# Kernel optimization log

Measured on AMD Instinct MI355X. Metric: run time of the kernel, lower is better.

Reference implementation:

```python
import jax, jax.numpy as jnp
import numpy as np

HEADS = 8
DIM_HEAD = 64


def setup_inputs() -> dict:
    key = jax.random.key(0)
    ks = jax.random.split(key, 7)
    b, c, h, w = 8, 256, 64, 64
    hidden = HEADS * DIM_HEAD  # 512
    return {
        "x": jax.random.normal(ks[0], (b, c, h, w), dtype=jnp.float32),
        "context": jax.random.normal(ks[1], (b, c, h, w), dtype=jnp.float32),
        "Wq": jax.random.normal(ks[2], (hidden, c), dtype=jnp.float32) * 0.02,
        "Wk": jax.random.normal(ks[3], (hidden, c), dtype=jnp.float32) * 0.02,
        "Wv": jax.random.normal(ks[4], (hidden, c), dtype=jnp.float32) * 0.02,
        "Wo": jax.random.normal(ks[5], (c, hidden), dtype=jnp.float32) * 0.02,
        "bo": jnp.zeros((c,), dtype=jnp.float32),
    }


def reference(x, context, Wq, Wk, Wv, Wo, bo):
    b, c, h, w = x.shape
    n = h * w
    scale = DIM_HEAD ** (-0.5)
    xf = x.reshape(b, c, n)                      # b c n
    cf = context.reshape(b, context.shape[1], -1)  # b c m
    # 1x1 convs == per-pixel linear projections
    q = jnp.einsum('bcn,oc->bon', xf, Wq).reshape(b, HEADS, DIM_HEAD, n) * scale
    k = jnp.einsum('bcm,oc->bom', cf, Wk).reshape(b, HEADS, DIM_HEAD, -1)
    v = jnp.einsum('bcm,oc->bom', cf, Wv).reshape(b, HEADS, DIM_HEAD, -1)
    k = jax.nn.softmax(k, axis=-1)               # softmax over spatial positions
    ctx = jnp.einsum('bhdm,bhem->bhde', k, v)    # small d x e context
    out = jnp.einsum('bhde,bhdn->bhen', ctx, q)  # b h e n
    out = out.reshape(b, HEADS * DIM_HEAD, h, w)
    return jnp.einsum('bchw,oc->bohw', out, Wo) + bo[None, :, None, None]
```

## Files before the change

### kernel.cpp

```cpp
#include <hip/hip_runtime.h>

#define B   8
#define C   256
#define N   4096
#define H   8
#define D   64
#define HID 512
#define SCALE 0.125f

typedef __attribute__((ext_vector_type(8))) __bf16 bf16x8;
typedef __attribute__((ext_vector_type(4))) float f32x4;

__device__ __forceinline__ ushort f2bf(float f) {
  union { float f; unsigned u; } v; v.f = f;
  unsigned r = v.u + 0x7FFFu + ((v.u >> 16) & 1u);
  return (ushort)(r >> 16);
}

__device__ __forceinline__ f32x4 mfma16(bf16x8 a, bf16x8 b, f32x4 c) {
  return __builtin_amdgcn_mfma_f32_16x16x32_bf16(a, b, c, 0, 0, 0);
}

__device__ __forceinline__ void glds16(const ushort* g, ushort* l) {
  __builtin_amdgcn_global_load_lds(
      (const __attribute__((address_space(1))) void*)g,
      (__attribute__((address_space(3))) void*)l, 16, 0, 0);
}

__global__ __launch_bounds__(256) void prep_kernel(
    const float* __restrict__ x, const float* __restrict__ ctxt,
    const float* __restrict__ Wk, const float* __restrict__ Wv,
    ushort* __restrict__ x_bf, ushort* __restrict__ ctxt_bf,
    ushort* __restrict__ wk_bf, ushort* __restrict__ wv_bf) {
  const int z = blockIdx.z;
  if (z == 16) {
    const int id = blockIdx.y * 64 + blockIdx.x;
    if (id >= 128) return;
    const int t = (id * 256 + threadIdx.x) * 4;
    const float4 a = *(const float4*)(Wk + t);
    const float4 b = *(const float4*)(Wv + t);
    ushort4 ra, rb;
    ra.x = f2bf(a.x); ra.y = f2bf(a.y); ra.z = f2bf(a.z); ra.w = f2bf(a.w);
    rb.x = f2bf(b.x); rb.y = f2bf(b.y); rb.z = f2bf(b.z); rb.w = f2bf(b.w);
    *(ushort4*)(wk_bf + t) = ra;
    *(ushort4*)(wv_bf + t) = rb;
    return;
  }
  __shared__ float tile[64 * 65];
  const int b = z & 7;
  const float* src = (z < 8) ? ctxt : x;
  ushort* dst = (z < 8) ? ctxt_bf : x_bf;
  const int l0 = blockIdx.x * 64, r0 = blockIdx.y * 64;
  const int tid = threadIdx.x;
  const int rr = tid >> 4, c4 = (tid & 15) << 2;
  const float* sp = src + ((size_t)b * C + r0) * N + l0;
#pragma unroll
  for (int p = 0; p < 4; ++p) {
    const float4 v = *(const float4*)(sp + (size_t)(rr + p * 16) * N + c4);
    float* tp = tile + (rr + p * 16) * 65 + c4;
    tp[0] = v.x; tp[1] = v.y; tp[2] = v.z; tp[3] = v.w;
  }
  __syncthreads();
  const int lr = tid >> 2, rb = (tid & 3) << 4;
  uint pk[8];
#pragma unroll
  for (int k = 0; k < 16; k += 2) {
    const uint lo = f2bf(tile[(rb + k) * 65 + lr]);
    const uint hi = f2bf(tile[(rb + k + 1) * 65 + lr]);
    pk[k >> 1] = lo | (hi << 16);
  }
  ushort* dp = dst + ((size_t)b * N + l0 + lr) * C + r0 + rb;
  *(uint4*)dp = *(uint4*)pk;
  *(uint4*)(dp + 8) = *(uint4*)(pk + 4);
}

__global__ __launch_bounds__(256, 4) void kv_mfma_kernel(
    const ushort* __restrict__ ctxt_bf,
    const ushort* __restrict__ wk_bf,
    const ushort* __restrict__ wv_bf,
    float* __restrict__ ctx_part,
    float* __restrict__ z_part)
{
  __shared__ __align__(16) ushort cb_s[2][32 * 256];
  __shared__ __align__(16) ushort p_s[64 * 32];
  __shared__ __align__(16) ushort v_s[64 * 32];
  const int mt = blockIdx.x, h = blockIdx.y, b = blockIdx.z;
  const int tid = threadIdx.x;
  const int w = tid >> 6, lane = tid & 63;
  const int col = lane & 15, quad = lane >> 4;
  const int dw = w * 16;
  const int swc = (col & 3) ^ ((col >> 2) & 3);

  const ushort* wkp = wk_bf + (size_t)(h * 64 + dw + col) * C + quad * 8;
  const ushort* wvp = wv_bf + (size_t)(h * 64 + dw + col) * C + quad * 8;
  const ushort* cbase = ctxt_bf + ((size_t)b * N + (size_t)mt * 256) * C;

  const int grow0 = w * 8 + (lane >> 5);
  const int ggran = lane & 31;

  const f32x4 z4 = {0.f, 0.f, 0.f, 0.f};
  f32x4 cacc[4];
#pragma unroll
  for (int j = 0; j < 4; ++j) cacc[j] = z4;
  float zl = 0.f;

#pragma unroll
  for (int it = 0; it < 4; ++it) {
    const int row = grow0 + it * 2;
    glds16(cbase + (size_t)row * C + ((ggran ^ (row & 7)) << 3),
           &cb_s[0][(w * 8 + it * 2) * 256]);
  }
  __syncthreads();

  for (int t = 0; t < 8; ++t) {
    const int cur = t & 1;
    if (t < 7) {
      const ushort* nb = cbase + (size_t)(t + 1) * 32 * C;
#pragma unroll
      for (int it = 0; it < 4; ++it) {
        const int row = grow0 + it * 2;
        glds16(nb + (size_t)row * C + ((ggran ^ (row & 7)) << 3),
               &cb_s[cur ^ 1][(w * 8 + it * 2) * 256]);
      }
    }

    f32x4 kacc[2], vacc[2];
#pragma unroll
    for (int i = 0; i < 2; ++i) { kacc[i] = z4; vacc[i] = z4; }
#pragma unroll
    for (int kk = 0; kk < 8; ++kk) {
      bf16x8 a[2];
#pragma unroll
      for (int i = 0; i < 2; ++i) {
        const int r = i * 16 + col;
        a[i] = *(const bf16x8*)(&cb_s[cur][r * 256 +
                  ((((kk << 2) + quad) ^ (r & 7)) << 3)]);
      }
      const bf16x8 wkf = *(const bf16x8*)(wkp + (size_t)kk * 32);
      const bf16x8 wvf = *(const bf16x8*)(wvp + (size_t)kk * 32);
#pragma unroll
      for (int i = 0; i < 2; ++i) {
        kacc[i] = mfma16(a[i], wkf, kacc[i]);
        vacc[i] = mfma16(a[i], wvf, vacc[i]);
      }
    }

#pragma unroll
    for (int i = 0; i < 2; ++i) {
      const int off = (dw + col) * 32 +
                      (((i * 2 + (quad >> 1)) ^ swc) << 3) + ((quad & 1) << 2);
      const f32x4 k4 = kacc[i];
      const float e0 = __expf(k4[0]), e1 = __expf(k4[1]);
      const float e2 = __expf(k4[2]), e3 = __expf(k4[3]);
      zl += (e0 + e1) + (e2 + e3);
      ushort4 pk; pk.x = f2bf(e0); pk.y = f2bf(e1);
      pk.z = f2bf(e2); pk.w = f2bf(e3);
      *(ushort4*)(p_s + off) = pk;
      const f32x4 v4 = vacc[i];
      ushort4 vk; vk.x = f2bf(v4[0]); vk.y = f2bf(v4[1]);
      vk.z = f2bf(v4[2]); vk.w = f2bf(v4[3]);
      *(ushort4*)(v_s + off) = vk;
    }
    __syncthreads();

    {
      const int g = (quad ^ swc) << 3;
      const bf16x8 pa = *(const bf16x8*)(p_s + (dw + col) * 32 + g);
      bf16x8 vb[4];
#pragma unroll
      for (int j = 0; j < 4; ++j)
        vb[j] = *(const bf16x8*)(v_s + (j * 16 + col) * 32 + g);
#pragma unroll
      for (int j = 0; j < 4; ++j) cacc[j] = mfma16(pa, vb[j], cacc[j]);
    }
    __syncthreads();
  }

  {
    float s = zl;
    s += __shfl_xor(s, 16); s += __shfl_xor(s, 32);
    if (quad == 0)
      z_part[((size_t)(b * H + h) * 16 + mt) * 64 + dw + col] = s;
  }

  float* outp = ctx_part + ((size_t)(b * H + h) * 16 + mt) * 4096;
#pragma unroll
  for (int j = 0; j < 4; ++j)
#pragma unroll
    for (int r = 0; r < 4; ++r)
      outp[(size_t)(dw + quad * 4 + r) * 64 + j * 16 + col] = cacc[j][r];
}

__global__ __launch_bounds__(256) void combine_kernel(
    const float* __restrict__ ctx_part, const float* __restrict__ z_part,
    float* __restrict__ ctxn)
{
  const int bh = blockIdx.x, seg = blockIdx.y, tid = threadIdx.x;
  __shared__ float zs[64];
  if (tid < 64) {
    float z = 0.f;
#pragma unroll
    for (int p = 0; p < 16; ++p) z += z_part[((size_t)bh * 16 + p) * 64 + tid];
    zs[tid] = SCALE / z;
  }
  __syncthreads();
  const int idx = (seg << 8) + tid;
  const float* cp = ctx_part + (size_t)bh * 16 * 4096;
  float s = 0.f;
#pragma unroll
  for (int p = 0; p < 16; ++p) s += cp[(size_t)p * 4096 + idx];
  ctxn[((size_t)bh << 12) + idx] = s * zs[idx >> 6];
}

__global__ __launch_bounds__(256) void a_kernel(
    const float* __restrict__ ctxn, const float* __restrict__ Wq,
    float* __restrict__ A)
{
  const int bh = blockIdx.x, cti = blockIdx.y, tid = threadIdx.x;
  const int b = bh >> 3, h = bh & 7;
  const int c0 = cti << 6;
  __shared__ float ct[64 * 65];
  __shared__ float wq[64 * 68];
  for (int r = 0; r < 16; ++r) {
    const int idx = tid + (r << 8);
    ct[(idx & 63) * 65 + (idx >> 6)] = ctxn[((size_t)bh << 12) + idx];
    wq[(idx >> 6) * 68 + (idx & 63)] =
        Wq[(size_t)(h * 64 + (idx >> 6)) * C + c0 + (idx & 63)];
  }
  __syncthreads();
  const int e = tid & 63, co = tid >> 6;
  float acc[16];
#pragma unroll
  for (int k = 0; k < 16; ++k) acc[k] = 0.f;
  for (int d = 0; d < 64; ++d) {
    const float cv = ct[e * 65 + d];
    const float* wr = wq + d * 68 + co * 16;
#pragma unroll
    for (int k = 0; k < 16; ++k) acc[k] += cv * wr[k];
  }
  float* Ar = A + ((size_t)b * HID + h * 64 + e) * C + c0 + co * 16;
#pragma unroll
  for (int k = 0; k < 16; ++k) Ar[k] = acc[k];
}

__global__ __launch_bounds__(256) void m_kernel(
    const float* __restrict__ A, const float* __restrict__ Wo,
    ushort* __restrict__ M_bf)
{
  const int tile = blockIdx.x, b = blockIdx.y;
  const int o0 = (tile & 7) << 5, c0 = (tile >> 3) << 6;
  const int tid = threadIdx.x, tx = tid & 15, ty = tid >> 4;
  __shared__ float wo_s[16 * 36];
  __shared__ float a_s[16 * 68];
  float acc[2][4] = {{0.f}};
  const int ow = tid >> 3, koff = (tid & 7) << 1;
  const int kk = tid >> 4, cc = (tid & 15) << 2;
  for (int k0 = 0; k0 < HID; k0 += 16) {
    __syncthreads();
    const float2 w2 = *(const float2*)(Wo + (size_t)(o0 + ow) * HID + k0 + koff);
    wo_s[(koff + 0) * 36 + ow] = w2.x;
    wo_s[(koff + 1) * 36 + ow] = w2.y;
    *(float4*)(a_s + kk * 68 + cc) =
        *(const float4*)(A + ((size_t)b * HID + k0 + kk) * C + c0 + cc);
    __syncthreads();
#pragma unroll
    for (int kc = 0; kc < 16; ++kc) {
      const float2 wv = *(const float2*)(wo_s + kc * 36 + ty * 2);
      const float4 av = *(const float4*)(a_s + kc * 68 + tx * 4);
      acc[0][0] += wv.x * av.x; acc[0][1] += wv.x * av.y;
      acc[0][2] += wv.x * av.z; acc[0][3] += wv.x * av.w;
      acc[1][0] += wv.y * av.x; acc[1][1] += wv.y * av.y;
      acc[1][2] += wv.y * av.z; acc[1][3] += wv.y * av.w;
    }
  }
#pragma unroll
  for (int i = 0; i < 2; ++i) {
    ushort4 r;
    r.x = f2bf(acc[i][0]); r.y = f2bf(acc[i][1]);
    r.z = f2bf(acc[i][2]); r.w = f2bf(acc[i][3]);
    *(ushort4*)(M_bf + ((size_t)b * C + o0 + ty * 2 + i) * C + c0 + tx * 4) = r;
  }
}

__global__ __launch_bounds__(256, 4) void out_mfma_kernel(
    const ushort* __restrict__ M_bf,
    const ushort* __restrict__ x_bf,
    const float* __restrict__ bo, float* __restrict__ out)
{
  const int nt = blockIdx.x, ot = blockIdx.y, b = blockIdx.z;
  const int tid = threadIdx.x;
  const int w = tid >> 6, lane = tid & 63;
  const int col = lane & 15, quad = lane >> 4;
  const int o0 = ot * 32;
  const size_t n_base = (size_t)nt * 256 + w * 64;
  const ushort* Ab = M_bf + ((size_t)b * C + o0 + col) * C + quad * 8;
  const ushort* Bb = x_bf + ((size_t)b * N + n_base) * C + quad * 8;

  const f32x4 z4 = {0.f, 0.f, 0.f, 0.f};
  f32x4 acc[2][4];
#pragma unroll
  for (int i = 0; i < 2; ++i)
#pragma unroll
    for (int j = 0; j < 4; ++j) acc[i][j] = z4;

#pragma unroll
  for (int kk = 0; kk < 8; ++kk) {
    bf16x8 af[2], bfz[4];
#pragma unroll
    for (int i = 0; i < 2; ++i)
      af[i] = *(const bf16x8*)(Ab + (size_t)(i * 16) * C + kk * 32);
#pragma unroll
    for (int j = 0; j < 4; ++j)
      bfz[j] = *(const bf16x8*)(Bb + (size_t)(j * 16 + col) * C + kk * 32);
#pragma unroll
    for (int i = 0; i < 2; ++i)
#pragma unroll
      for (int j = 0; j < 4; ++j) acc[i][j] = mfma16(af[i], bfz[j], acc[i][j]);
  }

#pragma unroll
  for (int i = 0; i < 2; ++i)
#pragma unroll
    for (int r = 0; r < 4; ++r) {
      const int o = o0 + i * 16 + quad * 4 + r;
      const float bias = bo[o];
      float* op = out + ((size_t)b * C + o) * N + n_base + col;
#pragma unroll
      for (int j = 0; j < 4; ++j) op[j * 16] = acc[i][j][r] + bias;
    }
}

extern "C" void kernel_launch(void* const* d_in, const int* in_sizes, int n_in,
                              void* d_out, int out_size, void* d_ws, size_t ws_size,
                              hipStream_t stream) {
  const float* x    = (const float*)d_in[0];
  const float* ctxt = (const float*)d_in[1];
  const float* Wq   = (const float*)d_in[2];
  const float* Wk   = (const float*)d_in[3];
  const float* Wv   = (const float*)d_in[4];
  const float* Wo   = (const float*)d_in[5];
  const float* bo   = (const float*)d_in[6];
  float* out = (float*)d_out;

  char* p = (char*)d_ws;
  ushort* ctxt_bf = (ushort*)p;  p += (size_t)B * N * C * 2;
  ushort* x_bf    = (ushort*)p;  p += (size_t)B * N * C * 2;
  ushort* wk_bf   = (ushort*)p;  p += (size_t)HID * C * 2;
  ushort* wv_bf   = (ushort*)p;  p += (size_t)HID * C * 2;
  ushort* M_bf    = (ushort*)p;  p += (size_t)B * C * C * 2;
  float*  z_part  = (float*)p;   p += (size_t)B * H * 16 * 64 * 4;
  float*  ctxn    = (float*)p;   p += (size_t)B * H * D * D * 4;
  float*  ctx_part= (float*)p;   p += (size_t)B * H * 16 * 4096 * 4;
  float*  A       = ctx_part;

  prep_kernel<<<dim3(N / 64, C / 64, 17), 256, 0, stream>>>(
      x, ctxt, Wk, Wv, x_bf, ctxt_bf, wk_bf, wv_bf);
  kv_mfma_kernel<<<dim3(16, H, B), 256, 0, stream>>>(ctxt_bf, wk_bf, wv_bf, ctx_part, z_part);
  combine_kernel<<<dim3(B * H, 16), 256, 0, stream>>>(ctx_part, z_part, ctxn);
  a_kernel<<<dim3(B * H, 4), 256, 0, stream>>>(ctxn, Wq, A);
  m_kernel<<<dim3(32, B), 256, 0, stream>>>(A, Wo, M_bf);
  out_mfma_kernel<<<dim3(N / 256, C / 32, B), 256, 0, stream>>>(M_bf, x_bf, bo, out);
}
```

Before: 218.0 us.

## Replace combine pass with atomics, hoist weight fragments, pipeline m_kernel, use native bf16 cast

The partial-context combine kernel is removed. kv_mfma blocks now atomically accumulate into a zeroed ctxn and z_sum, the zeroing is folded into prep_kernel, and the softmax normalization moves into a_kernel. Wk/Wv fragments are hoisted into registers once per block, MFMA sections get raised wave priority, and m_kernel uses 64-wide k tiles with register prefetch. The manual bf16 rounding is replaced by a compiler cast. The changes save one launch and the partial-buffer traffic, at the cost of atomic contention, nondeterministic summation order and more register pressure.

```diff
diff --git a/kernel.cpp b/kernel.cpp
--- a/kernel.cpp
+++ b/kernel.cpp
@@ -11,10 +11,8 @@
 typedef __attribute__((ext_vector_type(8))) __bf16 bf16x8;
 typedef __attribute__((ext_vector_type(4))) float f32x4;
 
-__device__ __forceinline__ ushort f2bf(float f) {
-  union { float f; unsigned u; } v; v.f = f;
-  unsigned r = v.u + 0x7FFFu + ((v.u >> 16) & 1u);
-  return (ushort)(r >> 16);
+__device__ __forceinline__ ushort bfbits(float f) {
+  union { __bf16 h; ushort u; } c; c.h = (__bf16)f; return c.u;
 }
 
 __device__ __forceinline__ f32x4 mfma16(bf16x8 a, bf16x8 b, f32x4 c) {
@@ -31,19 +29,28 @@
     const float* __restrict__ x, const float* __restrict__ ctxt,
     const float* __restrict__ Wk, const float* __restrict__ Wv,
     ushort* __restrict__ x_bf, ushort* __restrict__ ctxt_bf,
-    ushort* __restrict__ wk_bf, ushort* __restrict__ wv_bf) {
+    ushort* __restrict__ wk_bf, ushort* __restrict__ wv_bf,
+    float* __restrict__ ctxn, float* __restrict__ z_sum) {
   const int z = blockIdx.z;
+  const int tid = threadIdx.x;
   if (z == 16) {
     const int id = blockIdx.y * 64 + blockIdx.x;
-    if (id >= 128) return;
-    const int t = (id * 256 + threadIdx.x) * 4;
-    const float4 a = *(const float4*)(Wk + t);
-    const float4 b = *(const float4*)(Wv + t);
-    ushort4 ra, rb;
-    ra.x = f2bf(a.x); ra.y = f2bf(a.y); ra.z = f2bf(a.z); ra.w = f2bf(a.w);
-    rb.x = f2bf(b.x); rb.y = f2bf(b.y); rb.z = f2bf(b.z); rb.w = f2bf(b.w);
-    *(ushort4*)(wk_bf + t) = ra;
-    *(ushort4*)(wv_bf + t) = rb;
+    if (id < 128) {
+      const int t = (id * 256 + tid) * 4;
+      const float4 a = *(const float4*)(Wk + t);
+      const float4 b = *(const float4*)(Wv + t);
+      ushort4 ra, rb;
+      ra.x = bfbits(a.x); ra.y = bfbits(a.y); ra.z = bfbits(a.z); ra.w = bfbits(a.w);
+      rb.x = bfbits(b.x); rb.y = bfbits(b.y); rb.z = bfbits(b.z); rb.w = bfbits(b.w);
+      *(ushort4*)(wk_bf + t) = ra;
+      *(ushort4*)(wv_bf + t) = rb;
+    } else {
+      const int zb = id - 128;
+      const float4 zz = {0.f, 0.f, 0.f, 0.f};
+      *(float4*)(ctxn + (size_t)(zb * 512 + tid) * 4) = zz;
+      *(float4*)(ctxn + (size_t)(zb * 512 + 256 + tid) * 4) = zz;
+      if (zb < 4) *(float4*)(z_sum + (size_t)(zb * 256 + tid) * 4) = zz;
+    }
     return;
   }
   __shared__ float tile[64 * 65];
@@ -51,7 +58,6 @@
   const float* src = (z < 8) ? ctxt : x;
   ushort* dst = (z < 8) ? ctxt_bf : x_bf;
   const int l0 = blockIdx.x * 64, r0 = blockIdx.y * 64;
-  const int tid = threadIdx.x;
   const int rr = tid >> 4, c4 = (tid & 15) << 2;
   const float* sp = src + ((size_t)b * C + r0) * N + l0;
 #pragma unroll
@@ -65,8 +71,8 @@
   uint pk[8];
 #pragma unroll
   for (int k = 0; k < 16; k += 2) {
-    const uint lo = f2bf(tile[(rb + k) * 65 + lr]);
-    const uint hi = f2bf(tile[(rb + k + 1) * 65 + lr]);
+    const uint lo = bfbits(tile[(rb + k) * 65 + lr]);
+    const uint hi = bfbits(tile[(rb + k + 1) * 65 + lr]);
     pk[k >> 1] = lo | (hi << 16);
   }
   ushort* dp = dst + ((size_t)b * N + l0 + lr) * C + r0 + rb;
@@ -78,8 +84,8 @@
     const ushort* __restrict__ ctxt_bf,
     const ushort* __restrict__ wk_bf,
     const ushort* __restrict__ wv_bf,
-    float* __restrict__ ctx_part,
-    float* __restrict__ z_part)
+    float* __restrict__ ctxn,
+    float* __restrict__ z_sum)
 {
   __shared__ __align__(16) ushort cb_s[2][32 * 256];
   __shared__ __align__(16) ushort p_s[64 * 32];
@@ -95,6 +101,13 @@
   const ushort* wvp = wv_bf + (size_t)(h * 64 + dw + col) * C + quad * 8;
   const ushort* cbase = ctxt_bf + ((size_t)b * N + (size_t)mt * 256) * C;
 
+  bf16x8 wkf[8], wvf[8];
+#pragma unroll
+  for (int kk = 0; kk < 8; ++kk) {
+    wkf[kk] = *(const bf16x8*)(wkp + (size_t)kk * 32);
+    wvf[kk] = *(const bf16x8*)(wvp + (size_t)kk * 32);
+  }
+
   const int grow0 = w * 8 + (lane >> 5);
   const int ggran = lane & 31;
 
@@ -127,6 +140,7 @@
     f32x4 kacc[2], vacc[2];
 #pragma unroll
     for (int i = 0; i < 2; ++i) { kacc[i] = z4; vacc[i] = z4; }
+    __builtin_amdgcn_s_setprio(1);
 #pragma unroll
     for (int kk = 0; kk < 8; ++kk) {
       bf16x8 a[2];
@@ -136,14 +150,13 @@
         a[i] = *(const bf16x8*)(&cb_s[cur][r * 256 +
                   ((((kk << 2) + quad) ^ (r & 7)) << 3)]);
       }
-      const bf16x8 wkf = *(const bf16x8*)(wkp + (size_t)kk * 32);
-      const bf16x8 wvf = *(const bf16x8*)(wvp + (size_t)kk * 32);
 #pragma unroll
       for (int i = 0; i < 2; ++i) {
-        kacc[i] = mfma16(a[i], wkf, kacc[i]);
-        vacc[i] = mfma16(a[i], wvf, vacc[i]);
+        kacc[i] = mfma16(a[i], wkf[kk], kacc[i]);
+        vacc[i] = mfma16(a[i], wvf[kk], vacc[i]);
       }
     }
+    __builtin_amdgcn_s_setprio(0);
 
 #pragma unroll
     for (int i = 0; i < 2; ++i) {
@@ -153,12 +166,12 @@
       const float e0 = __expf(k4[0]), e1 = __expf(k4[1]);
       const float e2 = __expf(k4[2]), e3 = __expf(k4[3]);
       zl += (e0 + e1) + (e2 + e3);
-      ushort4 pk; pk.x = f2bf(e0); pk.y = f2bf(e1);
-      pk.z = f2bf(e2); pk.w = f2bf(e3);
+      ushort4 pk; pk.x = bfbits(e0); pk.y = bfbits(e1);
+      pk.z = bfbits(e2); pk.w = bfbits(e3);
       *(ushort4*)(p_s + off) = pk;
       const f32x4 v4 = vacc[i];
-      ushort4 vk; vk.x = f2bf(v4[0]); vk.y = f2bf(v4[1]);
-      vk.z = f2bf(v4[2]); vk.w = f2bf(v4[3]);
+      ushort4 vk; vk.x = bfbits(v4[0]); vk.y = bfbits(v4[1]);
+      vk.z = bfbits(v4[2]); vk.w = bfbits(v4[3]);
       *(ushort4*)(v_s + off) = vk;
     }
     __syncthreads();
@@ -170,8 +183,10 @@
 #pragma unroll
       for (int j = 0; j < 4; ++j)
         vb[j] = *(const bf16x8*)(v_s + (j * 16 + col) * 32 + g);
+      __builtin_amdgcn_s_setprio(1);
 #pragma unroll
       for (int j = 0; j < 4; ++j) cacc[j] = mfma16(pa, vb[j], cacc[j]);
+      __builtin_amdgcn_s_setprio(0);
     }
     __syncthreads();
   }
@@ -180,47 +195,29 @@
     float s = zl;
     s += __shfl_xor(s, 16); s += __shfl_xor(s, 32);
     if (quad == 0)
-      z_part[((size_t)(b * H + h) * 16 + mt) * 64 + dw + col] = s;
-  }
-
-  float* outp = ctx_part + ((size_t)(b * H + h) * 16 + mt) * 4096;
+      atomicAdd(&z_sum[(size_t)(b * H + h) * 64 + dw + col], s);
+  }
+
+  float* outp = ctxn + (size_t)(b * H + h) * 4096;
 #pragma unroll
   for (int j = 0; j < 4; ++j)
 #pragma unroll
     for (int r = 0; r < 4; ++r)
-      outp[(size_t)(dw + quad * 4 + r) * 64 + j * 16 + col] = cacc[j][r];
-}
-
-__global__ __launch_bounds__(256) void combine_kernel(
-    const float* __restrict__ ctx_part, const float* __restrict__ z_part,
-    float* __restrict__ ctxn)
-{
-  const int bh = blockIdx.x, seg = blockIdx.y, tid = threadIdx.x;
-  __shared__ float zs[64];
-  if (tid < 64) {
-    float z = 0.f;
-#pragma unroll
-    for (int p = 0; p < 16; ++p) z += z_part[((size_t)bh * 16 + p) * 64 + tid];
-    zs[tid] = SCALE / z;
-  }
-  __syncthreads();
-  const int idx = (seg << 8) + tid;
-  const float* cp = ctx_part + (size_t)bh * 16 * 4096;
-  float s = 0.f;
-#pragma unroll
-  for (int p = 0; p < 16; ++p) s += cp[(size_t)p * 4096 + idx];
-  ctxn[((size_t)bh << 12) + idx] = s * zs[idx >> 6];
+      atomicAdd(&outp[(size_t)(dw + quad * 4 + r) * 64 + j * 16 + col],
+                cacc[j][r]);
 }
 
 __global__ __launch_bounds__(256) void a_kernel(
-    const float* __restrict__ ctxn, const float* __restrict__ Wq,
-    float* __restrict__ A)
+    const float* __restrict__ ctxn, const float* __restrict__ z_sum,
+    const float* __restrict__ Wq, float* __restrict__ A)
 {
   const int bh = blockIdx.x, cti = blockIdx.y, tid = threadIdx.x;
   const int b = bh >> 3, h = bh & 7;
   const int c0 = cti << 6;
   __shared__ float ct[64 * 65];
   __shared__ float wq[64 * 68];
+  __shared__ float zs[64];
+  if (tid < 64) zs[tid] = SCALE / z_sum[(size_t)bh * 64 + tid];
   for (int r = 0; r < 16; ++r) {
     const int idx = tid + (r << 8);
     ct[(idx & 63) * 65 + (idx >> 6)] = ctxn[((size_t)bh << 12) + idx];
@@ -233,7 +230,7 @@
 #pragma unroll
   for (int k = 0; k < 16; ++k) acc[k] = 0.f;
   for (int d = 0; d < 64; ++d) {
-    const float cv = ct[e * 65 + d];
+    const float cv = ct[e * 65 + d] * zs[d];
     const float* wr = wq + d * 68 + co * 16;
 #pragma unroll
     for (int k = 0; k < 16; ++k) acc[k] += cv * wr[k];
@@ -250,22 +247,41 @@
   const int tile = blockIdx.x, b = blockIdx.y;
   const int o0 = (tile & 7) << 5, c0 = (tile >> 3) << 6;
   const int tid = threadIdx.x, tx = tid & 15, ty = tid >> 4;
-  __shared__ float wo_s[16 * 36];
-  __shared__ float a_s[16 * 68];
+  __shared__ float wo_s[64 * 33];
+  __shared__ float a_s[64 * 68];
   float acc[2][4] = {{0.f}};
-  const int ow = tid >> 3, koff = (tid & 7) << 1;
-  const int kk = tid >> 4, cc = (tid & 15) << 2;
-  for (int k0 = 0; k0 < HID; k0 += 16) {
+  const int wo_o = tid >> 3, wo_k = (tid & 7) << 3;
+  const int a_k = tid >> 2, a_c = (tid & 3) << 4;
+  float4 wr0, wr1, ar0, ar1, ar2, ar3;
+  {
+    const float* wp = Wo + (size_t)(o0 + wo_o) * HID + wo_k;
+    wr0 = *(const float4*)wp; wr1 = *(const float4*)(wp + 4);
+    const float* ap = A + ((size_t)b * HID + a_k) * C + c0 + a_c;
+    ar0 = *(const float4*)ap;       ar1 = *(const float4*)(ap + 4);
+    ar2 = *(const float4*)(ap + 8); ar3 = *(const float4*)(ap + 12);
+  }
+  for (int t = 0; t < 8; ++t) {
     __syncthreads();
-    const float2 w2 = *(const float2*)(Wo + (size_t)(o0 + ow) * HID + k0 + koff);
-    wo_s[(koff + 0) * 36 + ow] = w2.x;
-    wo_s[(koff + 1) * 36 + ow] = w2.y;
-    *(float4*)(a_s + kk * 68 + cc) =
-        *(const float4*)(A + ((size_t)b * HID + k0 + kk) * C + c0 + cc);
+    {
+      float* wd = wo_s + wo_k * 33 + wo_o;
+      wd[0]   = wr0.x; wd[33]  = wr0.y; wd[66]  = wr0.z; wd[99]  = wr0.w;
+      wd[132] = wr1.x; wd[165] = wr1.y; wd[198] = wr1.z; wd[231] = wr1.w;
+      float* ad = a_s + a_k * 68 + a_c;
+      *(float4*)ad = ar0;       *(float4*)(ad + 4) = ar1;
+      *(float4*)(ad + 8) = ar2; *(float4*)(ad + 12) = ar3;
+    }
     __syncthreads();
-#pragma unroll
-    for (int kc = 0; kc < 16; ++kc) {
-      const float2 wv = *(const float2*)(wo_s + kc * 36 + ty * 2);
+    if (t < 7) {
+      const int k0 = (t + 1) << 6;
+      const float* wp = Wo + (size_t)(o0 + wo_o) * HID + k0 + wo_k;
+      wr0 = *(const float4*)wp; wr1 = *(const float4*)(wp + 4);
+      const float* ap = A + ((size_t)b * HID + k0 + a_k) * C + c0 + a_c;
+      ar0 = *(const float4*)ap;       ar1 = *(const float4*)(ap + 4);
+      ar2 = *(const float4*)(ap + 8); ar3 = *(const float4*)(ap + 12);
+    }
+#pragma unroll
+    for (int kc = 0; kc < 64; ++kc) {
+      const float2 wv = *(const float2*)(wo_s + kc * 33 + ty * 2);
       const float4 av = *(const float4*)(a_s + kc * 68 + tx * 4);
       acc[0][0] += wv.x * av.x; acc[0][1] += wv.x * av.y;
       acc[0][2] += wv.x * av.z; acc[0][3] += wv.x * av.w;
@@ -276,8 +292,8 @@
 #pragma unroll
   for (int i = 0; i < 2; ++i) {
     ushort4 r;
-    r.x = f2bf(acc[i][0]); r.y = f2bf(acc[i][1]);
-    r.z = f2bf(acc[i][2]); r.w = f2bf(acc[i][3]);
+    r.x = bfbits(acc[i][0]); r.y = bfbits(acc[i][1]);
+    r.z = bfbits(acc[i][2]); r.w = bfbits(acc[i][3]);
     *(ushort4*)(M_bf + ((size_t)b * C + o0 + ty * 2 + i) * C + c0 + tx * 4) = r;
   }
 }
@@ -348,16 +364,15 @@
   ushort* wk_bf   = (ushort*)p;  p += (size_t)HID * C * 2;
   ushort* wv_bf   = (ushort*)p;  p += (size_t)HID * C * 2;
   ushort* M_bf    = (ushort*)p;  p += (size_t)B * C * C * 2;
-  float*  z_part  = (float*)p;   p += (size_t)B * H * 16 * 64 * 4;
+  float*  z_sum   = (float*)p;   p += (size_t)B * H * 64 * 4;
   float*  ctxn    = (float*)p;   p += (size_t)B * H * D * D * 4;
-  float*  ctx_part= (float*)p;   p += (size_t)B * H * 16 * 4096 * 4;
-  float*  A       = ctx_part;
+  float*  A       = (float*)p;   p += (size_t)B * HID * C * 4;
 
   prep_kernel<<<dim3(N / 64, C / 64, 17), 256, 0, stream>>>(
-      x, ctxt, Wk, Wv, x_bf, ctxt_bf, wk_bf, wv_bf);
-  kv_mfma_kernel<<<dim3(16, H, B), 256, 0, stream>>>(ctxt_bf, wk_bf, wv_bf, ctx_part, z_part);
-  combine_kernel<<<dim3(B * H, 16), 256, 0, stream>>>(ctx_part, z_part, ctxn);
-  a_kernel<<<dim3(B * H, 4), 256, 0, stream>>>(ctxn, Wq, A);
+      x, ctxt, Wk, Wv, x_bf, ctxt_bf, wk_bf, wv_bf, ctxn, z_sum);
+  kv_mfma_kernel<<<dim3(16, H, B), 256, 0, stream>>>(
+      ctxt_bf, wk_bf, wv_bf, ctxn, z_sum);
+  a_kernel<<<dim3(B * H, 4), 256, 0, stream>>>(ctxn, z_sum, Wq, A);
   m_kernel<<<dim3(32, B), 256, 0, stream>>>(A, Wo, M_bf);
   out_mfma_kernel<<<dim3(N / 256, C / 32, B), 256, 0, stream>>>(M_bf, x_bf, bo, out);
 }
```

Result: slower. 236.0 us (+8.3%).
